# Kernel optimization log

Measured on AMD Instinct MI355X. Metric: run time of the kernel, lower is better.

Reference implementation:

```python
import jax, jax.numpy as jnp
import numpy as np


def setup_inputs() -> dict:
    key = jax.random.key(0)
    ks = jax.random.split(key, 5)
    B, N, L, d = 8, 2048, 2048, 512
    q = N // 4
    return {
        "logits": jax.random.normal(ks[0], (B, N, L), jnp.float32),
        "emb0": jax.random.normal(ks[1], (q, d), jnp.float32),
        "emb1": jax.random.normal(ks[2], (q, d), jnp.float32),
        "emb2": jax.random.normal(ks[3], (q, d), jnp.float32),
        "emb3": jax.random.normal(ks[4], (q, d), jnp.float32),
    }


def reference(logits, emb0, emb1, emb2, emb3):
    # Eval / late-epoch path of Embedding.forward (process_block_max, k=3):
    # per head: top-k over codebook dim -> masked softmax -> einsum combine.
    # softmax over only the top-k values is mathematically identical to
    # softmax of the -inf-masked full logits, and gathering the k codebook
    # rows is identical to the dense einsum 'bnl,nm->bml' with that sparse attn.
    K = 3
    B, N, L = logits.shape
    E = jnp.stack([emb0, emb1, emb2, emb3])            # (4, q, d)
    q = E.shape[1]
    lg = logits.reshape(B, 4, q, L).transpose(0, 1, 3, 2)  # (B, 4, L, q)
    vals, idx = jax.lax.top_k(lg, K)                   # (B, 4, L, K)
    w = jax.nn.softmax(vals, axis=-1)                  # sparse attn weights

    def head(emb_h, idx_h, w_h):
        g = emb_h[idx_h]                               # (B, L, K, d) gather
        return jnp.einsum('blk,blkd->bld', w_h, g)     # (B, L, d)

    outs = jax.vmap(head, in_axes=(0, 1, 1))(E, idx, w)  # (4, B, L, d)
    # output = out_0 + out_1 + out_2 + out_3, returned as (B, d, L)
    return outs.sum(axis=0).transpose(0, 2, 1)
```

## Files before the change

### kernel.cpp

```cpp
#include <hip/hip_runtime.h>
#include <math.h>

#define BB 8
#define NN 2048
#define LL 2048
#define QQ 512
#define DD 512

typedef float f4 __attribute__((ext_vector_type(4)));

__device__ __forceinline__ void top3_insert(float v, int i, float& m0,
                                            float& m1, float& m2, int& j0,
                                            int& j1, int& j2) {
  bool gt0 = v > m0, gt1 = v > m1, gt2 = v > m2;
  float nv2 = gt1 ? m1 : (gt2 ? v : m2);
  int   ni2 = gt1 ? j1 : (gt2 ? i : j2);
  float nv1 = gt0 ? m0 : (gt1 ? v : m1);
  int   ni1 = gt0 ? j0 : (gt1 ? i : j1);
  m0 = gt0 ? v : m0;
  j0 = gt0 ? i : j0;
  m1 = nv1; j1 = ni1; m2 = nv2; j2 = ni2;
}

__device__ __forceinline__ unsigned bf16_rne(float f) {
  unsigned u = __float_as_uint(f);
  return (u + 0x7FFFu + ((u >> 16) & 1u)) >> 16;
}

__global__ __launch_bounds__(256) void cvt_kernel(
    const float* __restrict__ e0, const float* __restrict__ e1,
    const float* __restrict__ e2, const float* __restrict__ e3,
    unsigned short* __restrict__ ebf) {
  const float* embs[4] = {e0, e1, e2, e3};
  const int h = blockIdx.y;
  const int i = (blockIdx.x * 256 + threadIdx.x) * 8;
  const float* src = embs[h] + i;
  const float4 x = *(const float4*)src;
  const float4 y = *(const float4*)(src + 4);
  uint4 o;
  o.x = bf16_rne(x.x) | (bf16_rne(x.y) << 16);
  o.y = bf16_rne(x.z) | (bf16_rne(x.w) << 16);
  o.z = bf16_rne(y.x) | (bf16_rne(y.y) << 16);
  o.w = bf16_rne(y.z) | (bf16_rne(y.w) << 16);
  *(uint4*)(ebf + (size_t)h * QQ * DD + i) = o;
}

__global__ __launch_bounds__(256) void topk_part_kernel(
    const float* __restrict__ logits, f4* __restrict__ part) {
  const int u     = threadIdx.x & 63;
  const int g     = threadIdx.x >> 6;
  const int lt    = blockIdx.x;
  const int h     = blockIdx.y;
  const int b     = blockIdx.z >> 1;
  const int ns    = blockIdx.z & 1;
  const int chunk = ns * 4 + g;
  const int n0    = chunk * 64;
  const int l4    = lt * 256 + u * 4;

  const float* base = logits + ((size_t)(b * NN + h * QQ + n0) * LL) + l4;

  float v0[4], v1[4], v2[4];
  int   i0[4], i1[4], i2[4];
#pragma unroll
  for (int j = 0; j < 4; ++j) {
    v0[j] = v1[j] = v2[j] = -INFINITY;
    i0[j] = i1[j] = i2[j] = 0;
  }

  f4 buf[8];
  for (int t = 0; t < 8; ++t) {
#pragma unroll
    for (int p = 0; p < 8; ++p)
      buf[p] = __builtin_nontemporal_load(
          (const f4*)(base + (size_t)(t * 8 + p) * LL));
#pragma unroll
    for (int p = 0; p < 8; ++p) {
      const int i = n0 + t * 8 + p;
      top3_insert(buf[p][0], i, v0[0], v1[0], v2[0], i0[0], i1[0], i2[0]);
      top3_insert(buf[p][1], i, v0[1], v1[1], v2[1], i0[1], i1[1], i2[1]);
      top3_insert(buf[p][2], i, v0[2], v1[2], v2[2], i0[2], i1[2], i2[2]);
      top3_insert(buf[p][3], i, v0[3], v1[3], v2[3], i0[3], i1[3], i2[3]);
    }
  }

  f4* pout = part + ((size_t)((b * 4 + h) * 8 + chunk)) * LL + l4;
#pragma unroll
  for (int j = 0; j < 4; ++j) {
    unsigned int pi = (unsigned int)i0[j] | ((unsigned int)i1[j] << 9) |
                      ((unsigned int)i2[j] << 18);
    f4 rec = {v0[j], v1[j], v2[j], __uint_as_float(pi)};
    pout[j] = rec;
  }
}

__global__ __launch_bounds__(256) void combine_kernel(
    const f4* __restrict__ part, const unsigned short* __restrict__ ebf,
    float* __restrict__ out) {
  const int u    = threadIdx.x & 63;
  const int w    = threadIdx.x >> 6;
  const int lblk = blockIdx.x * 16;
  const int b    = blockIdx.y;

  __shared__ float wt_s[4][16][3];
  __shared__ int   rid_s[4][16][3];
  __shared__ float tile[16][516];

  if (threadIdx.x < 64) {
    const int h  = threadIdx.x >> 4;
    const int il = threadIdx.x & 15;
    const int l  = lblk + il;
    const f4* pp = part + ((size_t)(b * 4 + h) * 8) * LL + l;

    float m0 = -INFINITY, m1 = -INFINITY, m2 = -INFINITY;
    int   j0 = 0, j1 = 0, j2 = 0;
#pragma unroll
    for (int c = 0; c < 8; ++c) {
      const f4 P = __builtin_nontemporal_load(pp + (size_t)c * LL);
      unsigned int pi = __float_as_uint(P[3]);
      top3_insert(P[0], pi & 511, m0, m1, m2, j0, j1, j2);
      top3_insert(P[1], (pi >> 9) & 511, m0, m1, m2, j0, j1, j2);
      top3_insert(P[2], (pi >> 18) & 511, m0, m1, m2, j0, j1, j2);
    }
    float e1 = __expf(m1 - m0), e2 = __expf(m2 - m0);
    float inv = 1.0f / (1.0f + e1 + e2);
    wt_s[h][il][0] = inv;
    wt_s[h][il][1] = e1 * inv;
    wt_s[h][il][2] = e2 * inv;
    rid_s[h][il][0] = j0;
    rid_s[h][il][1] = j1;
    rid_s[h][il][2] = j2;
  }
  __syncthreads();

#pragma unroll
  for (int il = 0; il < 4; ++il) {
    const int ll = w * 4 + il;
    float wt[12];
    const unsigned short* rows[12];
#pragma unroll
    for (int h = 0; h < 4; ++h) {
#pragma unroll
      for (int k = 0; k < 3; ++k) {
        wt[h * 3 + k]   = wt_s[h][ll][k];
        rows[h * 3 + k] = ebf + ((size_t)h * QQ + rid_s[h][ll][k]) * DD;
      }
    }
#pragma unroll
    for (int p = 0; p < 2; ++p) {
      const int d = p * 256 + u * 4;
      float a0 = 0.f, a1 = 0.f, a2 = 0.f, a3 = 0.f;
#pragma unroll
      for (int m = 0; m < 12; ++m) {
        const uint2 e = *(const uint2*)(rows[m] + d);
        a0 += wt[m] * __uint_as_float(e.x << 16);
        a1 += wt[m] * __uint_as_float(e.x & 0xFFFF0000u);
        a2 += wt[m] * __uint_as_float(e.y << 16);
        a3 += wt[m] * __uint_as_float(e.y & 0xFFFF0000u);
      }
      *(float4*)&tile[ll][d] = make_float4(a0, a1, a2, a3);
    }
  }
  __syncthreads();

  const int l0  = (threadIdx.x & 3) * 4;
  const int dof = threadIdx.x >> 2;
  float* outb = out + (size_t)b * DD * LL + lblk + l0;
#pragma unroll
  for (int dd = 0; dd < 512; dd += 64) {
    const int d = dd + dof;
    f4 r;
    r[0] = tile[l0 + 0][d];
    r[1] = tile[l0 + 1][d];
    r[2] = tile[l0 + 2][d];
    r[3] = tile[l0 + 3][d];
    __builtin_nontemporal_store(r, (f4*)(outb + (size_t)d * LL));
  }
}

extern "C" void kernel_launch(void* const* d_in, const int* in_sizes, int n_in,
                              void* d_out, int out_size, void* d_ws,
                              size_t ws_size, hipStream_t stream) {
  const float* logits = (const float*)d_in[0];
  const float* emb0   = (const float*)d_in[1];
  const float* emb1   = (const float*)d_in[2];
  const float* emb2   = (const float*)d_in[3];
  const float* emb3   = (const float*)d_in[4];
  float*       out    = (float*)d_out;
  f4*          part   = (f4*)d_ws;
  unsigned short* ebf = (unsigned short*)((char*)d_ws + (8u << 20));

  dim3 gc(128, 4);
  cvt_kernel<<<gc, 256, 0, stream>>>(emb0, emb1, emb2, emb3, ebf);

  dim3 ga(8, 4, 16);
  topk_part_kernel<<<ga, 256, 0, stream>>>(logits, part);

  dim3 gb(LL / 16, BB);
  combine_kernel<<<gb, 256, 0, stream>>>(part, ebf, out);
}
```

Baseline: 214.1 us.

## Fuse bf16 codebook conversion into topk kernel and widen combine output tiles

The separate fp32-to-bf16 embedding conversion kernel is removed. Its work now runs in 32 extra blocks (blockIdx.z == 16) of the top-k partial kernel, which saves one launch and overlaps the conversion with the logits scan. The combine kernel now handles 32 L positions per 512-thread block and processes d in two halves of 256 through a smaller shared tile. That makes each output row write 32 contiguous floats instead of 16, at the cost of extra barriers.

```diff
diff --git a/kernel.cpp b/kernel.cpp
--- a/kernel.cpp
+++ b/kernel.cpp
@@ -27,26 +27,31 @@
   return (u + 0x7FFFu + ((u >> 16) & 1u)) >> 16;
 }
 
-__global__ __launch_bounds__(256) void cvt_kernel(
-    const float* __restrict__ e0, const float* __restrict__ e1,
-    const float* __restrict__ e2, const float* __restrict__ e3,
-    unsigned short* __restrict__ ebf) {
-  const float* embs[4] = {e0, e1, e2, e3};
-  const int h = blockIdx.y;
-  const int i = (blockIdx.x * 256 + threadIdx.x) * 8;
-  const float* src = embs[h] + i;
-  const float4 x = *(const float4*)src;
-  const float4 y = *(const float4*)(src + 4);
-  uint4 o;
-  o.x = bf16_rne(x.x) | (bf16_rne(x.y) << 16);
-  o.y = bf16_rne(x.z) | (bf16_rne(x.w) << 16);
-  o.z = bf16_rne(y.x) | (bf16_rne(y.y) << 16);
-  o.w = bf16_rne(y.z) | (bf16_rne(y.w) << 16);
-  *(uint4*)(ebf + (size_t)h * QQ * DD + i) = o;
-}
-
 __global__ __launch_bounds__(256) void topk_part_kernel(
-    const float* __restrict__ logits, f4* __restrict__ part) {
+    const float* __restrict__ logits, const float* __restrict__ e0,
+    const float* __restrict__ e1, const float* __restrict__ e2,
+    const float* __restrict__ e3, unsigned short* __restrict__ ebf,
+    f4* __restrict__ part) {
+  if (blockIdx.z == 16) {
+    const float* srcs[4] = {e0, e1, e2, e3};
+    const int fid = blockIdx.x + 8 * blockIdx.y;
+    const int h   = fid >> 3;
+    const float* src = srcs[h] + (fid & 7) * 32768;
+#pragma unroll
+    for (int k = 0; k < 16; ++k) {
+      const int off = k * 2048 + threadIdx.x * 8;
+      const float4 x = *(const float4*)(src + off);
+      const float4 y = *(const float4*)(src + off + 4);
+      uint4 o;
+      o.x = bf16_rne(x.x) | (bf16_rne(x.y) << 16);
+      o.y = bf16_rne(x.z) | (bf16_rne(x.w) << 16);
+      o.z = bf16_rne(y.x) | (bf16_rne(y.y) << 16);
+      o.w = bf16_rne(y.z) | (bf16_rne(y.w) << 16);
+      *(uint4*)(ebf + (size_t)h * QQ * DD + (fid & 7) * 32768 + off) = o;
+    }
+    return;
+  }
+
   const int u     = threadIdx.x & 63;
   const int g     = threadIdx.x >> 6;
   const int lt    = blockIdx.x;
@@ -93,21 +98,21 @@
   }
 }
 
-__global__ __launch_bounds__(256) void combine_kernel(
+__global__ __launch_bounds__(512) void combine_kernel(
     const f4* __restrict__ part, const unsigned short* __restrict__ ebf,
     float* __restrict__ out) {
   const int u    = threadIdx.x & 63;
   const int w    = threadIdx.x >> 6;
-  const int lblk = blockIdx.x * 16;
+  const int lblk = blockIdx.x * 32;
   const int b    = blockIdx.y;
 
-  __shared__ float wt_s[4][16][3];
-  __shared__ int   rid_s[4][16][3];
-  __shared__ float tile[16][516];
-
-  if (threadIdx.x < 64) {
-    const int h  = threadIdx.x >> 4;
-    const int il = threadIdx.x & 15;
+  __shared__ float wt_s[4][32][3];
+  __shared__ int   rid_s[4][32][3];
+  __shared__ float tile[32][260];
+
+  if (threadIdx.x < 128) {
+    const int h  = threadIdx.x >> 5;
+    const int il = threadIdx.x & 31;
     const int l  = lblk + il;
     const f4* pp = part + ((size_t)(b * 4 + h) * 8) * LL + l;
 
@@ -132,22 +137,26 @@
   }
   __syncthreads();
 
-#pragma unroll
-  for (int il = 0; il < 4; ++il) {
-    const int ll = w * 4 + il;
-    float wt[12];
-    const unsigned short* rows[12];
-#pragma unroll
-    for (int h = 0; h < 4; ++h) {
-#pragma unroll
-      for (int k = 0; k < 3; ++k) {
-        wt[h * 3 + k]   = wt_s[h][ll][k];
-        rows[h * 3 + k] = ebf + ((size_t)h * QQ + rid_s[h][ll][k]) * DD;
+  const int l0  = (threadIdx.x & 7) * 4;
+  const int dof = threadIdx.x >> 3;
+  float* outb = out + (size_t)b * DD * LL + lblk + l0;
+
+  for (int dh = 0; dh < 2; ++dh) {
+#pragma unroll
+    for (int il = 0; il < 4; ++il) {
+      const int ll = w * 4 + il;
+      float wt[12];
+      const unsigned short* rows[12];
+#pragma unroll
+      for (int h = 0; h < 4; ++h) {
+#pragma unroll
+        for (int k = 0; k < 3; ++k) {
+          wt[h * 3 + k] = wt_s[h][ll][k];
+          rows[h * 3 + k] =
+              ebf + ((size_t)h * QQ + rid_s[h][ll][k]) * DD + dh * 256;
+        }
       }
-    }
-#pragma unroll
-    for (int p = 0; p < 2; ++p) {
-      const int d = p * 256 + u * 4;
+      const int d = u * 4;
       float a0 = 0.f, a1 = 0.f, a2 = 0.f, a3 = 0.f;
 #pragma unroll
       for (int m = 0; m < 12; ++m) {
@@ -159,21 +168,18 @@
       }
       *(float4*)&tile[ll][d] = make_float4(a0, a1, a2, a3);
     }
-  }
-  __syncthreads();
-
-  const int l0  = (threadIdx.x & 3) * 4;
-  const int dof = threadIdx.x >> 2;
-  float* outb = out + (size_t)b * DD * LL + lblk + l0;
-#pragma unroll
-  for (int dd = 0; dd < 512; dd += 64) {
-    const int d = dd + dof;
-    f4 r;
-    r[0] = tile[l0 + 0][d];
-    r[1] = tile[l0 + 1][d];
-    r[2] = tile[l0 + 2][d];
-    r[3] = tile[l0 + 3][d];
-    __builtin_nontemporal_store(r, (f4*)(outb + (size_t)d * LL));
+    __syncthreads();
+#pragma unroll
+    for (int dd = 0; dd < 256; dd += 64) {
+      const int d = dd + dof;
+      f4 r;
+      r[0] = tile[l0 + 0][d];
+      r[1] = tile[l0 + 1][d];
+      r[2] = tile[l0 + 2][d];
+      r[3] = tile[l0 + 3][d];
+      __builtin_nontemporal_store(r, (f4*)(outb + (size_t)(dh * 256 + d) * LL));
+    }
+    __syncthreads();
   }
 }
 
@@ -189,12 +195,10 @@
   f4*          part   = (f4*)d_ws;
   unsigned short* ebf = (unsigned short*)((char*)d_ws + (8u << 20));
 
-  dim3 gc(128, 4);
-  cvt_kernel<<<gc, 256, 0, stream>>>(emb0, emb1, emb2, emb3, ebf);
-
-  dim3 ga(8, 4, 16);
-  topk_part_kernel<<<ga, 256, 0, stream>>>(logits, part);
-
-  dim3 gb(LL / 16, BB);
-  combine_kernel<<<gb, 256, 0, stream>>>(part, ebf, out);
-}
+  dim3 ga(8, 4, 17);
+  topk_part_kernel<<<ga, 256, 0, stream>>>(logits, emb0, emb1, emb2, emb3,
+                                           ebf, part);
+
+  dim3 gb(LL / 32, BB);
+  combine_kernel<<<gb, 512, 0, stream>>>(part, ebf, out);
+}
```

Measured after the change: 216.9 us. Within noise of the previous version (+1.3%).
